# Performance work log

Hardware: AMD Instinct MI355X
Metric: run time of the kernel (lower is better)

Reference implementation:

```python
import jax, jax.numpy as jnp
import numpy as np

NBITS = 8
QMAX = 2 ** (NBITS - 1) - 1  # 127
EPS_S = 1e-8


def ste_round(x):
    # straight-through estimator round (matches HAWQ ste_round)
    return x + jax.lax.stop_gradient(jnp.round(x) - x)


def quant_act(x):
    # symmetric per-tensor 8-bit fake quantization (QuantAct)
    s = jnp.maximum(jnp.max(jnp.abs(x)) / QMAX, EPS_S)
    xq = jnp.clip(ste_round(x / s), -QMAX - 1, QMAX)
    return xq * s, s


def quant_weight_per_channel(w, axis=0):
    # symmetric per-output-channel 8-bit fake quantization (weights)
    red = tuple(i for i in range(w.ndim) if i != axis)
    s = jnp.maximum(jnp.max(jnp.abs(w), axis=red, keepdims=True) / QMAX, EPS_S)
    wq = jnp.clip(ste_round(w / s), -QMAX - 1, QMAX)
    return wq * s, s


def setup_inputs() -> dict:
    key = jax.random.key(0)
    ks = jax.random.split(key, 6)
    B, Cin, Cout, H, W = 32, 256, 128, 56, 56
    x = jax.random.normal(ks[0], (B, Cin, H, W), jnp.float32)
    bn_gamma = 1.0 + 0.1 * jax.random.normal(ks[1], (Cin,), jnp.float32)
    bn_beta = 0.1 * jax.random.normal(ks[2], (Cin,), jnp.float32)
    bn_mean = 0.1 * jax.random.normal(ks[3], (Cin,), jnp.float32)
    bn_var = jax.random.uniform(ks[4], (Cin,), jnp.float32, minval=0.5, maxval=1.5)
    conv_w = jax.random.normal(ks[5], (Cout, Cin), jnp.float32) * (1.0 / np.sqrt(Cin))
    return {"x": x, "bn_gamma": bn_gamma, "bn_beta": bn_beta,
            "bn_mean": bn_mean, "bn_var": bn_var, "conv_w": conv_w}


def reference(x, bn_gamma, bn_beta, bn_mean, bn_var, conv_w):
    bn_eps = 1e-5
    # --- QuantAct on incoming activations ---
    x, act_s = quant_act(x)
    # --- QuantBn: fold BN into per-channel scale/shift, quantize folded weight ---
    w_fold = bn_gamma * jax.lax.rsqrt(bn_var + bn_eps)        # [Cin]
    b_fold = bn_beta - bn_mean * w_fold                       # [Cin]
    wq, bn_s = quant_weight_per_channel(w_fold, axis=0)
    x = x * wq[None, :, None, None] + b_fold[None, :, None, None]
    # --- QuantAct1: requantize post-BN output (act_s * bn_s threaded) ---
    x, act_s = quant_act(x)
    # --- ReLU ---
    x = jax.nn.relu(x)
    # --- QuantConv2d: 1x1 conv, per-output-channel quantized weight ---
    cwq, conv_s = quant_weight_per_channel(conv_w, axis=0)    # [Cout, Cin]
    x = jnp.einsum('bchw,oc->bohw', x, cwq)                   # [B, Cout, H, W]
    # --- QuantAct2: requantize post-conv output ---
    x, act_s = quant_act(x)
    # --- QuantAveragePool2d(2,2): pool in integer domain, rescale back ---
    B, C, H, W = x.shape
    x_int = x / act_s
    pooled = x_int.reshape(B, C, H // 2, 2, W // 2, 2).mean(axis=(3, 5))
    x = pooled * act_s
    # --- QuantAct3 ---
    x, act_s = quant_act(x)
    return x, act_s
```

## Files before the change

kernel.cpp:

```cpp
#include <hip/hip_runtime.h>
#include <math.h>

#define QMAXF 127.0f
#define EPSF  1e-8f
#define CIN   256
#define COUT  128
#define HW    3136
#define W_    56
#define NPOOL 3211264
#define POOL_BLOCKS 1792

typedef unsigned short u16;
typedef unsigned int   u32;
typedef __attribute__((ext_vector_type(8))) short s16x8;
typedef __attribute__((ext_vector_type(4))) float f32x4;

#define WQ_OFF   8
#define BF_OFF   264
#define EMAX_OFF 520
#define EMIN_OFF 776
#define CS_OFF   1032
#define CWB_OFF  1160
#define Y_OFF    17544

__device__ __forceinline__ float qclip(float v) {
    return fminf(fmaxf(v, -128.0f), 127.0f);
}
__device__ __forceinline__ u16 bf16bits(float f) {
    return (u16)(__float_as_uint(f) >> 16);
}
__device__ __forceinline__ u32 encf(float f) {
    u32 u = __float_as_uint(f);
    return (u & 0x80000000u) ? ~u : (u | 0x80000000u);
}
__device__ __forceinline__ float decf(u32 k) {
    return __uint_as_float((k & 0x80000000u) ? (k ^ 0x80000000u) : ~k);
}

__device__ __forceinline__ void block_max_atomic(float v, float* red, u32* dst) {
    #pragma unroll
    for (int off = 32; off > 0; off >>= 1) v = fmaxf(v, __shfl_xor(v, off));
    const int lane = threadIdx.x & 63, wid = threadIdx.x >> 6;
    if (lane == 0) red[wid] = v;
    __syncthreads();
    if (threadIdx.x == 0) {
        const int nw = blockDim.x >> 6;
        float m = red[0];
        for (int i = 1; i < nw; ++i) m = fmaxf(m, red[i]);
        atomicMax(dst, __float_as_uint(m));
    }
}

__global__ void k0w(const float* __restrict__ cw, float* __restrict__ ws) {
    const int t = threadIdx.x;
    if (blockIdx.x == COUT) {
        ((u32*)ws)[EMAX_OFF + t] = 0u;
        ((u32*)ws)[EMIN_OFF + t] = 0xFFFFFFFFu;
        if (t < 2) ((u32*)ws)[2 + t] = 0u;
        return;
    }
    __shared__ float red[4];
    const int o = blockIdx.x;
    const float wv = cw[o * CIN + t];
    float v = fabsf(wv);
    #pragma unroll
    for (int off = 32; off > 0; off >>= 1) v = fmaxf(v, __shfl_xor(v, off));
    if ((t & 63) == 0) red[t >> 6] = v;
    __syncthreads();
    const float mx = fmaxf(fmaxf(red[0], red[1]), fmaxf(red[2], red[3]));
    const float s = fmaxf(mx / QMAXF, EPSF);
    const float q = qclip(rintf(wv / s));
    ((u16*)(ws + CWB_OFF))[o * CIN + t] = bf16bits(q);
    if (t == 0) ws[CS_OFF + o] = s;
}

__global__ void k1_minmax(const float* __restrict__ x, float* __restrict__ ws) {
    __shared__ float red[8];
    const int row = blockIdx.x;
    const float4* xr = (const float4*)(x + (size_t)row * HW);
    float mx = -3.402823466e38f, mn = 3.402823466e38f;
    for (int i = threadIdx.x; i < HW / 4; i += 256) {
        const float4 v = xr[i];
        mx = fmaxf(mx, fmaxf(fmaxf(v.x, v.y), fmaxf(v.z, v.w)));
        mn = fminf(mn, fminf(fminf(v.x, v.y), fminf(v.z, v.w)));
    }
    #pragma unroll
    for (int off = 32; off > 0; off >>= 1) {
        mx = fmaxf(mx, __shfl_xor(mx, off));
        mn = fminf(mn, __shfl_xor(mn, off));
    }
    if ((threadIdx.x & 63) == 0) {
        red[threadIdx.x >> 6] = mx;
        red[4 + (threadIdx.x >> 6)] = mn;
    }
    __syncthreads();
    if (threadIdx.x == 0) {
        mx = fmaxf(fmaxf(red[0], red[1]), fmaxf(red[2], red[3]));
        mn = fminf(fminf(red[4], red[5]), fminf(red[6], red[7]));
        const int c = row & (CIN - 1);
        atomicMax((u32*)ws + EMAX_OFF + c, encf(mx));
        atomicMin((u32*)ws + EMIN_OFF + c, encf(mn));
    }
}

__global__ void k0b(const float* __restrict__ g, const float* __restrict__ be,
                    const float* __restrict__ mnp, const float* __restrict__ vr,
                    float* __restrict__ ws) {
    __shared__ float red[4];
    __shared__ float s1sh;
    const int t = threadIdx.x;
    const float cmax = decf(((u32*)ws)[EMAX_OFF + t]);
    const float cmin = decf(((u32*)ws)[EMIN_OFF + t]);
    float v = fmaxf(fabsf(cmax), fabsf(cmin));
    #pragma unroll
    for (int off = 32; off > 0; off >>= 1) v = fmaxf(v, __shfl_xor(v, off));
    if ((t & 63) == 0) red[t >> 6] = v;
    __syncthreads();
    if (t == 0) {
        const float m1 = fmaxf(fmaxf(red[0], red[1]), fmaxf(red[2], red[3]));
        ws[0] = m1;
        s1sh = fmaxf(m1 / QMAXF, EPSF);
    }
    __syncthreads();
    const float s1 = s1sh;
    const float wf = g[t] / sqrtf(vr[t] + 1e-5f);
    const float bf = be[t] - mnp[t] * wf;
    const float sw = fmaxf(fabsf(wf) / QMAXF, EPSF);
    const float q  = qclip(rintf(wf / sw));
    const float wqd = __fmul_rn(q, sw);
    ws[WQ_OFF + t] = wqd;
    ws[BF_OFF + t] = bf;
    const float q1h = qclip(rintf(cmax / s1));
    const float q1l = qclip(rintf(cmin / s1));
    const float xh = __fadd_rn(__fmul_rn(__fmul_rn(q1h, s1), wqd), bf);
    const float xl = __fadd_rn(__fmul_rn(__fmul_rn(q1l, s1), wqd), bf);
    float m2 = fmaxf(fabsf(xh), fabsf(xl));
    __syncthreads();
    #pragma unroll
    for (int off = 32; off > 0; off >>= 1) m2 = fmaxf(m2, __shfl_xor(m2, off));
    if ((t & 63) == 0) red[t >> 6] = m2;
    __syncthreads();
    if (t == 0) ws[1] = fmaxf(fmaxf(red[0], red[1]), fmaxf(red[2], red[3]));
}

__global__ __launch_bounds__(256) void k3_mfma(const float* __restrict__ x,
                                               float* __restrict__ ws) {
    __shared__ __align__(16) u16 Xs[64 * 64];
    __shared__ __align__(16) u16 Wt[128 * 64];
    __shared__ float Wqs[CIN], Bfs[CIN], Css[COUT];
    __shared__ float red[4];

    const int t   = threadIdx.x;
    const int b   = blockIdx.x / 49;
    const int hw0 = (blockIdx.x % 49) * 64;
    const int l   = t & 63, w = t >> 6;
    const int wc  = (w >> 1) * 64;
    const int wp  = (w & 1) * 32;

    const float s1 = fmaxf(ws[0] / QMAXF, EPSF);
    const float s2 = fmaxf(ws[1] / QMAXF, EPSF);

    Wqs[t] = ws[WQ_OFF + t];
    Bfs[t] = ws[BF_OFF + t];
    if (t < COUT) Css[t] = ws[CS_OFF + t];
    __syncthreads();

    f32x4 acc[4][2];
    #pragma unroll
    for (int m = 0; m < 4; ++m)
        #pragma unroll
        for (int n = 0; n < 2; ++n) acc[m][n] = (f32x4)0.0f;

    const u16* cwb = (const u16*)(ws + CWB_OFF);
    const int px0 = (t & 15) * 4;
    const int kx  = t >> 4;

    for (int ck = 0; ck < CIN; ck += 64) {
        #pragma unroll
        for (int ps = 0; ps < 4; ++ps) {
            const int c = ck + ps * 16 + kx;
            const float4 xv = *(const float4*)(x + ((size_t)(b * CIN + c)) * HW + hw0 + px0);
            const float wqc = Wqs[c], bfc = Bfs[c];
            const int kloc = ps * 16 + kx;
            const float vv[4] = {xv.x, xv.y, xv.z, xv.w};
            #pragma unroll
            for (int u = 0; u < 4; ++u) {
                const int p = px0 + u;
                const float q1 = qclip(rintf(vv[u] / s1));
                const float xd = __fmul_rn(q1, s1);
                const float x2 = __fadd_rn(__fmul_rn(xd, wqc), bfc);
                const float q2 = qclip(rintf(x2 / s2));
                const float a  = fmaxf(q2, 0.0f);
                Xs[p * 64 + ((((kloc >> 3) + p + (p >> 3)) & 7) * 8) + (kloc & 7)] = bf16bits(a);
            }
        }
        #pragma unroll
        for (int ps = 0; ps < 4; ++ps) {
            const int o  = ps * 32 + (t >> 3);
            const int kk = (t & 7) * 8;
            const s16x8 wv = *(const s16x8*)(cwb + o * CIN + ck + kk);
            *(s16x8*)&Wt[o * 64 + ((((kk >> 3) + o + (o >> 3)) & 7) * 8)] = wv;
        }
        __syncthreads();
        #pragma unroll
        for (int ks = 0; ks < 2; ++ks) {
            const int ch = ks * 4 + (l >> 4);
            s16x8 xf[2], wfr[4];
            #pragma unroll
            for (int n = 0; n < 2; ++n) {
                const int p = wp + n * 16 + (l & 15);
                xf[n] = *(const s16x8*)&Xs[p * 64 + (((ch + p + (p >> 3)) & 7) * 8)];
            }
            #pragma unroll
            for (int m = 0; m < 4; ++m) {
                const int o = wc + m * 16 + (l & 15);
                wfr[m] = *(const s16x8*)&Wt[o * 64 + (((ch + o + (o >> 3)) & 7) * 8)];
            }
            #pragma unroll
            for (int m = 0; m < 4; ++m)
                #pragma unroll
                for (int n = 0; n < 2; ++n)
                    acc[m][n] = __builtin_amdgcn_mfma_f32_16x16x32_bf16(
                                    wfr[m], xf[n], acc[m][n], 0, 0, 0);
        }
        __syncthreads();
    }

    float mloc = 0.0f;
    #pragma unroll
    for (int m = 0; m < 4; ++m) {
        #pragma unroll
        for (int n = 0; n < 2; ++n) {
            const int pix = hw0 + wp + n * 16 + (l & 15);
            #pragma unroll
            for (int r = 0; r < 4; ++r) {
                const int o = wc + m * 16 + (l >> 4) * 4 + r;
                const float sc = __fmul_rn(s2, Css[o]);
                const float val = __fmul_rn(acc[m][n][r], sc);
                ws[Y_OFF + ((size_t)(b * COUT + o)) * HW + pix] = val;
                mloc = fmaxf(mloc, fabsf(val));
            }
        }
    }
    block_max_atomic(mloc, red, (u32*)ws + 2);
}

__global__ void k4_pool(float* __restrict__ ws, float* __restrict__ out) {
    __shared__ float red[4];
    const float s3 = fmaxf(ws[2] / QMAXF, EPSF);
    float mloc = 0.0f;
    const int nq2 = NPOOL / 2;
    for (int p = blockIdx.x * 256 + threadIdx.x; p < nq2;
         p += POOL_BLOCKS * 256) {
        const int j2  = p % 14;
        const int tmp = p / 14;
        const int i   = tmp % 28;
        const int bo  = tmp / 28;
        const float* yb = ws + Y_OFF + (size_t)bo * HW + (2 * i) * W_ + 4 * j2;
        const float4 r0 = *(const float4*)yb;
        const float4 r1 = *(const float4*)(yb + W_);
        const float q00 = qclip(rintf(r0.x / s3)), q01 = qclip(rintf(r0.y / s3));
        const float q02 = qclip(rintf(r0.z / s3)), q03 = qclip(rintf(r0.w / s3));
        const float q10 = qclip(rintf(r1.x / s3)), q11 = qclip(rintf(r1.y / s3));
        const float q12 = qclip(rintf(r1.z / s3)), q13 = qclip(rintf(r1.w / s3));
        const float p0 = __fmul_rn(__fmul_rn((q00 + q01) + (q10 + q11), 0.25f), s3);
        const float p1 = __fmul_rn(__fmul_rn((q02 + q03) + (q12 + q13), 0.25f), s3);
        float2 pv; pv.x = p0; pv.y = p1;
        *(float2*)(out + (size_t)bo * 784 + i * 28 + 2 * j2) = pv;
        mloc = fmaxf(mloc, fmaxf(fabsf(p0), fabsf(p1)));
    }
    block_max_atomic(mloc, red, (u32*)ws + 3);
}

__global__ void k5_final(float* __restrict__ out, const float* __restrict__ ws) {
    const float s4 = fmaxf(ws[3] / QMAXF, EPSF);
    const int n4 = NPOOL / 4;
    for (int i = blockIdx.x * 256 + threadIdx.x; i < n4; i += 3136 * 256) {
        float4 v = *(float4*)(out + 4 * (size_t)i);
        v.x = __fmul_rn(qclip(rintf(v.x / s4)), s4);
        v.y = __fmul_rn(qclip(rintf(v.y / s4)), s4);
        v.z = __fmul_rn(qclip(rintf(v.z / s4)), s4);
        v.w = __fmul_rn(qclip(rintf(v.w / s4)), s4);
        *(float4*)(out + 4 * (size_t)i) = v;
    }
    if (blockIdx.x == 0 && threadIdx.x == 0) out[NPOOL] = s4;
}

extern "C" void kernel_launch(void* const* d_in, const int* in_sizes, int n_in,
                              void* d_out, int out_size, void* d_ws, size_t ws_size,
                              hipStream_t stream) {
    const float* x     = (const float*)d_in[0];
    const float* gamma = (const float*)d_in[1];
    const float* beta  = (const float*)d_in[2];
    const float* mean  = (const float*)d_in[3];
    const float* var   = (const float*)d_in[4];
    const float* cw    = (const float*)d_in[5];
    float* out = (float*)d_out;
    float* ws  = (float*)d_ws;

    hipLaunchKernelGGL(k0w, dim3(COUT + 1), dim3(256), 0, stream, cw, ws);
    hipLaunchKernelGGL(k1_minmax, dim3(32 * CIN), dim3(256), 0, stream, x, ws);
    hipLaunchKernelGGL(k0b, dim3(1), dim3(256), 0, stream, gamma, beta, mean, var, ws);
    hipLaunchKernelGGL(k3_mfma, dim3(1568), dim3(256), 0, stream, x, ws);
    hipLaunchKernelGGL(k4_pool, dim3(POOL_BLOCKS), dim3(256), 0, stream, ws, out);
    hipLaunchKernelGGL(k5_final, dim3(3136), dim3(256), 0, stream, out, ws);
}
```

Baseline: 139.9 us.

## Double-buffer LDS tiles and prefetch next K-chunk into registers in conv GEMM

The 1x1 conv MFMA kernel now keeps two LDS buffers for the activation and weight tiles. It loads the next 64-channel chunk of x and weights into registers before running the MFMAs on the current buffer, then transforms and stores that chunk into the other buffer. This hides global load latency behind compute and halves the barriers per K step. The x load pattern also changes from float4 per thread to scalar loads with one pixel per thread, so each thread packs bf16 pairs and writes 16-byte LDS stores instead of scattered 2-byte stores. The cost is more registers (16 floats plus 4 vectors) and twice the LDS, which may lower occupancy.

```diff
diff --git a/kernel.cpp b/kernel.cpp
--- a/kernel.cpp
+++ b/kernel.cpp
@@ -49,6 +49,15 @@
         for (int i = 1; i < nw; ++i) m = fmaxf(m, red[i]);
         atomicMax(dst, __float_as_uint(m));
     }
+}
+
+__device__ __forceinline__ float xform(float xv, float s1, float s2,
+                                       float wqc, float bfc) {
+    const float q1 = qclip(rintf(xv / s1));
+    const float xd = __fmul_rn(q1, s1);
+    const float x2 = __fadd_rn(__fmul_rn(xd, wqc), bfc);
+    const float q2 = qclip(rintf(x2 / s2));
+    return fmaxf(q2, 0.0f);
 }
 
 __global__ void k0w(const float* __restrict__ cw, float* __restrict__ ws) {
@@ -143,10 +152,37 @@
     if (t == 0) ws[1] = fmaxf(fmaxf(red[0], red[1]), fmaxf(red[2], red[3]));
 }
 
+__device__ __forceinline__ void stage_store(u16* __restrict__ Xb, u16* __restrict__ Wb,
+                                            const float* __restrict__ xr,
+                                            const s16x8* __restrict__ wreg,
+                                            int t, int ck, float s1, float s2,
+                                            const float* __restrict__ Wqs,
+                                            const float* __restrict__ Bfs) {
+    const int p = t & 63, kh = t >> 6;
+    u32 pk[8];
+    #pragma unroll
+    for (int j = 0; j < 8; ++j) {
+        const int c0 = ck + kh * 16 + 2 * j;
+        const float a0 = xform(xr[2 * j],     s1, s2, Wqs[c0],     Bfs[c0]);
+        const float a1 = xform(xr[2 * j + 1], s1, s2, Wqs[c0 + 1], Bfs[c0 + 1]);
+        pk[j] = (__float_as_uint(a0) >> 16) | (__float_as_uint(a1) & 0xFFFF0000u);
+    }
+    const int g0 = kh * 2;
+    uint4 v0; v0.x = pk[0]; v0.y = pk[1]; v0.z = pk[2]; v0.w = pk[3];
+    uint4 v1; v1.x = pk[4]; v1.y = pk[5]; v1.z = pk[6]; v1.w = pk[7];
+    *(uint4*)&Xb[p * 64 + (((g0 + p + (p >> 3)) & 7) * 8)]     = v0;
+    *(uint4*)&Xb[p * 64 + (((g0 + 1 + p + (p >> 3)) & 7) * 8)] = v1;
+    #pragma unroll
+    for (int ps = 0; ps < 4; ++ps) {
+        const int o = ps * 32 + (t >> 3);
+        *(s16x8*)&Wb[o * 64 + ((((t & 7) + o + (o >> 3)) & 7) * 8)] = wreg[ps];
+    }
+}
+
 __global__ __launch_bounds__(256) void k3_mfma(const float* __restrict__ x,
                                                float* __restrict__ ws) {
-    __shared__ __align__(16) u16 Xs[64 * 64];
-    __shared__ __align__(16) u16 Wt[128 * 64];
+    __shared__ __align__(16) u16 Xs[2][64 * 64];
+    __shared__ __align__(16) u16 Wt[2][128 * 64];
     __shared__ float Wqs[CIN], Bfs[CIN], Css[COUT];
     __shared__ float red[4];
 
@@ -163,7 +199,21 @@
     Wqs[t] = ws[WQ_OFF + t];
     Bfs[t] = ws[BF_OFF + t];
     if (t < COUT) Css[t] = ws[CS_OFF + t];
-    __syncthreads();
+
+    const u16* cwb = (const u16*)(ws + CWB_OFF);
+    const int p  = t & 63;
+    const int kh = t >> 6;
+    const float* xb = x + (size_t)b * CIN * HW + hw0 + p;
+
+    float xr[16];
+    s16x8 wreg[4];
+
+    #pragma unroll
+    for (int ps = 0; ps < 4; ++ps)
+        wreg[ps] = *(const s16x8*)(cwb + (ps * 32 + (t >> 3)) * CIN + (t & 7) * 8);
+    #pragma unroll
+    for (int j = 0; j < 16; ++j)
+        xr[j] = xb[(kh * 16 + j) * HW];
 
     f32x4 acc[4][2];
     #pragma unroll
@@ -171,50 +221,36 @@
         #pragma unroll
         for (int n = 0; n < 2; ++n) acc[m][n] = (f32x4)0.0f;
 
-    const u16* cwb = (const u16*)(ws + CWB_OFF);
-    const int px0 = (t & 15) * 4;
-    const int kx  = t >> 4;
-
-    for (int ck = 0; ck < CIN; ck += 64) {
-        #pragma unroll
-        for (int ps = 0; ps < 4; ++ps) {
-            const int c = ck + ps * 16 + kx;
-            const float4 xv = *(const float4*)(x + ((size_t)(b * CIN + c)) * HW + hw0 + px0);
-            const float wqc = Wqs[c], bfc = Bfs[c];
-            const int kloc = ps * 16 + kx;
-            const float vv[4] = {xv.x, xv.y, xv.z, xv.w};
-            #pragma unroll
-            for (int u = 0; u < 4; ++u) {
-                const int p = px0 + u;
-                const float q1 = qclip(rintf(vv[u] / s1));
-                const float xd = __fmul_rn(q1, s1);
-                const float x2 = __fadd_rn(__fmul_rn(xd, wqc), bfc);
-                const float q2 = qclip(rintf(x2 / s2));
-                const float a  = fmaxf(q2, 0.0f);
-                Xs[p * 64 + ((((kloc >> 3) + p + (p >> 3)) & 7) * 8) + (kloc & 7)] = bf16bits(a);
-            }
+    __syncthreads();
+    stage_store(Xs[0], Wt[0], xr, wreg, t, 0, s1, s2, Wqs, Bfs);
+    __syncthreads();
+
+    #pragma unroll
+    for (int it = 0; it < 4; ++it) {
+        const int ckn = (it + 1) * 64;
+        if (it < 3) {
+            #pragma unroll
+            for (int ps = 0; ps < 4; ++ps)
+                wreg[ps] = *(const s16x8*)(cwb + (ps * 32 + (t >> 3)) * CIN + ckn + (t & 7) * 8);
+            #pragma unroll
+            for (int j = 0; j < 16; ++j)
+                xr[j] = xb[(ckn + kh * 16 + j) * HW];
         }
-        #pragma unroll
-        for (int ps = 0; ps < 4; ++ps) {
-            const int o  = ps * 32 + (t >> 3);
-            const int kk = (t & 7) * 8;
-            const s16x8 wv = *(const s16x8*)(cwb + o * CIN + ck + kk);
-            *(s16x8*)&Wt[o * 64 + ((((kk >> 3) + o + (o >> 3)) & 7) * 8)] = wv;
-        }
-        __syncthreads();
+        const u16* Xb = Xs[it & 1];
+        const u16* Wb = Wt[it & 1];
         #pragma unroll
         for (int ks = 0; ks < 2; ++ks) {
             const int ch = ks * 4 + (l >> 4);
             s16x8 xf[2], wfr[4];
             #pragma unroll
             for (int n = 0; n < 2; ++n) {
-                const int p = wp + n * 16 + (l & 15);
-                xf[n] = *(const s16x8*)&Xs[p * 64 + (((ch + p + (p >> 3)) & 7) * 8)];
+                const int pp = wp + n * 16 + (l & 15);
+                xf[n] = *(const s16x8*)&Xb[pp * 64 + (((ch + pp + (pp >> 3)) & 7) * 8)];
             }
             #pragma unroll
             for (int m = 0; m < 4; ++m) {
                 const int o = wc + m * 16 + (l & 15);
-                wfr[m] = *(const s16x8*)&Wt[o * 64 + (((ch + o + (o >> 3)) & 7) * 8)];
+                wfr[m] = *(const s16x8*)&Wb[o * 64 + (((ch + o + (o >> 3)) & 7) * 8)];
             }
             #pragma unroll
             for (int m = 0; m < 4; ++m)
@@ -223,6 +259,9 @@
                     acc[m][n] = __builtin_amdgcn_mfma_f32_16x16x32_bf16(
                                     wfr[m], xf[n], acc[m][n], 0, 0, 0);
         }
+        if (it < 3)
+            stage_store(Xs[(it + 1) & 1], Wt[(it + 1) & 1], xr, wreg, t, ckn,
+                        s1, s2, Wqs, Bfs);
         __syncthreads();
     }
 
@@ -250,10 +289,10 @@
     const float s3 = fmaxf(ws[2] / QMAXF, EPSF);
     float mloc = 0.0f;
     const int nq2 = NPOOL / 2;
-    for (int p = blockIdx.x * 256 + threadIdx.x; p < nq2;
-         p += POOL_BLOCKS * 256) {
-        const int j2  = p % 14;
-        const int tmp = p / 14;
+    for (int pp = blockIdx.x * 256 + threadIdx.x; pp < nq2;
+         pp += POOL_BLOCKS * 256) {
+        const int j2  = pp % 14;
+        const int tmp = pp / 14;
         const int i   = tmp % 28;
         const int bo  = tmp / 28;
         const float* yb = ws + Y_OFF + (size_t)bo * HW + (2 * i) * W_ + 4 * j2;
```

After: 127.4 us. -8.9%, faster.
